# Kernel optimization log

Measured on AMD Instinct MI355X. Metric: run time of the kernel, lower is better.

## Reference

```python
import jax, jax.numpy as jnp
import numpy as np

N_NODES = 50000
N_EDGES = 800000
D_FEAT = 128
HIDDEN = 256
N_CLASSES = 2


def setup_inputs() -> dict:
    key = jax.random.key(0)
    ks = jax.random.split(key, 9)
    x = jax.random.normal(ks[0], (N_NODES, D_FEAT), dtype=jnp.float32)
    edge_index = jax.random.randint(ks[1], (2, N_EDGES), 0, N_NODES, dtype=jnp.int32)
    # SAGEConv params: lin_l (applied to aggregated neighbors), lin_r (root), bias
    s1 = 1.0 / np.sqrt(D_FEAT)
    s2 = 1.0 / np.sqrt(HIDDEN)
    W1l = jax.random.normal(ks[2], (D_FEAT, HIDDEN), dtype=jnp.float32) * s1
    W1r = jax.random.normal(ks[3], (D_FEAT, HIDDEN), dtype=jnp.float32) * s1
    b1 = jax.random.normal(ks[4], (HIDDEN,), dtype=jnp.float32) * s1
    W2l = jax.random.normal(ks[5], (HIDDEN, N_CLASSES), dtype=jnp.float32) * s2
    W2r = jax.random.normal(ks[6], (HIDDEN, N_CLASSES), dtype=jnp.float32) * s2
    b2 = jax.random.normal(ks[7], (N_CLASSES,), dtype=jnp.float32) * s2
    return {"x": x, "edge_index": edge_index, "W1l": W1l, "W1r": W1r,
            "b1": b1, "W2l": W2l, "W2r": W2r, "b2": b2}


def _sage_conv(x, src, dst, Wl, Wr, b):
    # mean-aggregate neighbor features x[src] into destination nodes
    n = x.shape[0]
    agg = jax.ops.segment_sum(x[src], dst, num_segments=n)  # [N, d]
    deg = jax.ops.segment_sum(jnp.ones((src.shape[0],), x.dtype), dst,
                              num_segments=n)
    mean = agg / jnp.maximum(deg, 1.0)[:, None]
    return mean @ Wl + x @ Wr + b


def reference(x, edge_index, W1l, W1r, b1, W2l, W2r, b2):
    src, dst = edge_index[0], edge_index[1]
    h = jax.nn.relu(_sage_conv(x, src, dst, W1l, W1r, b1))
    embeddings = h  # dropout is identity in eval mode
    out = jax.nn.sigmoid(_sage_conv(embeddings, src, dst, W2l, W2r, b2))
    return out, embeddings
```

## Files before the change

### kernel.cpp

```cpp
#include <hip/hip_runtime.h>
#include <math.h>

#define N_NODES 50000
#define N_EDGES 800000
#define D_FEAT 128
#define HIDDEN 256
#define NB_SCAN 196
#define GEMM_BLOCKS 1563

#define PREP_CVT_B 512
#define PREP_WF_B 64
#define AGG_B 2048

#define NSLICE 64
#define SLICE_E 12500
#define NPART 8
#define PART_N 6250

typedef __bf16 bf16x8 __attribute__((ext_vector_type(8)));
typedef float f32x4 __attribute__((ext_vector_type(4)));

__device__ __forceinline__ unsigned f2b(float f) {
    unsigned u = __builtin_bit_cast(unsigned, f);
    return (u + 0x7fff + ((u >> 16) & 1)) >> 16;
}

__global__ __launch_bounds__(256) void prep(
    const float* __restrict__ x,
    const float* __restrict__ W1l, const float* __restrict__ W1r,
    unsigned* __restrict__ xb, unsigned short* __restrict__ Wfrag) {
    int b = blockIdx.x;
    int t = threadIdx.x;
    if (b < PREP_CVT_B) {
        for (int g = b * 256 + t; g < 800000; g += PREP_CVT_B * 256) {
            float4 v0 = *(const float4*)(x + (size_t)g * 8);
            float4 v1 = *(const float4*)(x + (size_t)g * 8 + 4);
            uint4 o;
            o.x = f2b(v0.x) | (f2b(v0.y) << 16);
            o.y = f2b(v0.z) | (f2b(v0.w) << 16);
            o.z = f2b(v1.x) | (f2b(v1.y) << 16);
            o.w = f2b(v1.z) | (f2b(v1.w) << 16);
            int d = g >> 4;
            int j = (g & 15) << 2;
            *(uint4*)(xb + (size_t)d * 64 + j) = o;
        }
    } else {
        for (int tt = (b - PREP_CVT_B) * 256 + t; tt < 65536; tt += PREP_WF_B * 256) {
            int j = tt & 7;
            int lane = (tt >> 3) & 63;
            int ks = (tt >> 9) & 7;
            int nt = tt >> 12;
            int k = ks * 32 + ((lane >> 4) << 3) + j;
            int n = (nt << 4) + (lane & 15);
            float v = (k < 128) ? W1l[k * 256 + n] : W1r[(k - 128) * 256 + n];
            Wfrag[tt] = (unsigned short)f2b(v);
        }
    }
}

__global__ __launch_bounds__(1024) void hist_kernel(const int* __restrict__ dst,
                                                    unsigned* __restrict__ arr) {
    __shared__ unsigned hist[25000];
    int i = blockIdx.x;
    int t = threadIdx.x;
    for (int k = t; k < 25000; k += 1024) hist[k] = 0;
    __syncthreads();
    int e0 = i * SLICE_E;
    for (int k = t; k < SLICE_E; k += 1024) {
        int d = dst[e0 + k];
        atomicAdd(&hist[d >> 1], (d & 1) ? 65536u : 1u);
    }
    __syncthreads();
    for (int d = t; d < N_NODES; d += 1024)
        arr[(size_t)i * N_NODES + d] = (hist[d >> 1] >> ((d & 1) << 4)) & 0xffffu;
}

__global__ void scan1(const unsigned* __restrict__ arr, int* __restrict__ cnt,
                      int* __restrict__ bsum) {
    __shared__ int tmp[256];
    int t = threadIdx.x;
    int i = blockIdx.x * 256 + t;
    int c = 0;
    if (i < N_NODES) {
        for (int k = 0; k < NSLICE; k++) c += (int)arr[(size_t)k * N_NODES + i];
        cnt[i] = c;
    }
    tmp[t] = c;
    __syncthreads();
    for (int off = 128; off > 0; off >>= 1) {
        if (t < off) tmp[t] += tmp[t + off];
        __syncthreads();
    }
    if (t == 0) bsum[blockIdx.x] = tmp[0];
}

__global__ void scanB(const int* __restrict__ cnt, const int* __restrict__ bsum,
                      int* __restrict__ rowbeg, unsigned* __restrict__ arr) {
    __shared__ int bs[256];
    __shared__ int tmp[256];
    int t = threadIdx.x;
    int b = blockIdx.x;
    bs[t] = (t < NB_SCAN) ? bsum[t] : 0;
    __syncthreads();
    for (int off = 1; off < 256; off <<= 1) {
        int y = (t >= off) ? bs[t - off] : 0;
        __syncthreads();
        bs[t] += y;
        __syncthreads();
    }
    int boff = (b == 0) ? 0 : bs[b - 1];
    int i = b * 256 + t;
    int v = (i < N_NODES) ? cnt[i] : 0;
    tmp[t] = v;
    __syncthreads();
    for (int off = 1; off < 256; off <<= 1) {
        int y = (t >= off) ? tmp[t - off] : 0;
        __syncthreads();
        tmp[t] += y;
        __syncthreads();
    }
    if (i < N_NODES) {
        unsigned running = (unsigned)(tmp[t] - v + boff);
        rowbeg[i] = (int)running;
#pragma unroll 4
        for (int k = 0; k < NSLICE; k++) {
            unsigned old = arr[(size_t)k * N_NODES + i];
            arr[(size_t)k * N_NODES + i] = running;
            running += old;
        }
    }
}

__global__ __launch_bounds__(256) void scatter_kernel(
    const int* __restrict__ src, const int* __restrict__ dst,
    const unsigned* __restrict__ arr, unsigned short* __restrict__ esrc) {
    __shared__ unsigned off[PART_N];
    int g = blockIdx.x & 7;
    int i = blockIdx.x >> 3;
    int t = threadIdx.x;
    int lo = g * PART_N;
    for (int k = t; k < PART_N; k += 256)
        off[k] = arr[(size_t)i * N_NODES + lo + k];
    __syncthreads();
    int e0 = i * SLICE_E;
    for (int k = t; k < SLICE_E; k += 256) {
        int e = e0 + k;
        int d = dst[e];
        unsigned dl = (unsigned)(d - lo);
        if (dl < (unsigned)PART_N) {
            unsigned pos = atomicAdd(&off[dl], 1u);
            esrc[pos] = (unsigned short)src[e];
        }
    }
}

__global__ __launch_bounds__(256) void agg1(
    const unsigned* __restrict__ xb, unsigned* __restrict__ mb,
    const unsigned short* __restrict__ esrc,
    const int* __restrict__ rowbeg, const int* __restrict__ cnt) {
    int wid = (blockIdx.x * 256 + threadIdx.x) >> 6;
    int lane = threadIdx.x & 63;
    int g = lane >> 4;
    int i = lane & 15;
    for (int d = wid; d < N_NODES; d += AGG_B * 4) {
        int beg = rowbeg[d];
        int c = cnt[d];
        int end = beg + c;
        float acc[8];
#pragma unroll
        for (int f = 0; f < 8; f++) acc[f] = 0.0f;

        for (int base = beg; base < end; base += 64) {
            int m = end - base; if (m > 64) m = 64;
            int idx = base + lane;
            int e = (int)esrc[idx < end ? idx : end - 1];
            for (int j0 = 0; j0 < m; j0 += 4) {
                int ss = __shfl(e, j0 + g);
                float sc = (j0 + g < m) ? 1.0f : 0.0f;
                uint4 u = *(const uint4*)(xb + (size_t)ss * 64 + (i << 2));
                acc[0] += sc * __builtin_bit_cast(float, u.x << 16);
                acc[1] += sc * __builtin_bit_cast(float, u.x & 0xffff0000u);
                acc[2] += sc * __builtin_bit_cast(float, u.y << 16);
                acc[3] += sc * __builtin_bit_cast(float, u.y & 0xffff0000u);
                acc[4] += sc * __builtin_bit_cast(float, u.z << 16);
                acc[5] += sc * __builtin_bit_cast(float, u.z & 0xffff0000u);
                acc[6] += sc * __builtin_bit_cast(float, u.w << 16);
                acc[7] += sc * __builtin_bit_cast(float, u.w & 0xffff0000u);
            }
        }
#pragma unroll
        for (int f = 0; f < 8; f++) {
            acc[f] += __shfl_xor(acc[f], 16);
            acc[f] += __shfl_xor(acc[f], 32);
        }
        if (lane < 16) {
            float inv = 1.0f / fmaxf((float)c, 1.0f);
            uint4 o;
            o.x = f2b(acc[0] * inv) | (f2b(acc[1] * inv) << 16);
            o.y = f2b(acc[2] * inv) | (f2b(acc[3] * inv) << 16);
            o.z = f2b(acc[4] * inv) | (f2b(acc[5] * inv) << 16);
            o.w = f2b(acc[6] * inv) | (f2b(acc[7] * inv) << 16);
            *(uint4*)(mb + (size_t)d * 64 + (i << 2)) = o;
        }
    }
}

__global__ __launch_bounds__(256) void gemm1ps(
    const unsigned* __restrict__ mb, const unsigned* __restrict__ xb,
    const unsigned short* __restrict__ Wfrag, const float* __restrict__ b1,
    const float* __restrict__ W2l, const float* __restrict__ W2r,
    const float* __restrict__ b2,
    float* __restrict__ h, float* __restrict__ p, float* __restrict__ s) {
    __shared__ unsigned A[32 * 128];
    __shared__ float ppart[32][4];

    int r0 = blockIdx.x * 32;
    int tid = threadIdx.x;
    int w = tid >> 6;
    int lane = tid & 63;
    int quad = lane >> 4;
    int l15 = lane & 15;

    if (tid < 128) ((float*)ppart)[tid] = 0.0f;

    int sr = tid >> 3;
    int c0 = tid & 7;
#pragma unroll
    for (int j = 0; j < 4; j++) {
        int c = c0 + (j << 3);
        uint4 v;
        if (c < 16) v = *(const uint4*)(mb + (size_t)(r0 + sr) * 64 + (c << 2));
        else        v = *(const uint4*)(xb + (size_t)(r0 + sr) * 64 + ((c - 16) << 2));
        int cp = c ^ (sr & 7);
        *(uint4*)(A + sr * 128 + (cp << 2)) = v;
    }
    __syncthreads();

    f32x4 acc[8];
#pragma unroll
    for (int i = 0; i < 8; i++) acc[i] = (f32x4){0.0f, 0.0f, 0.0f, 0.0f};

    for (int ks = 0; ks < 8; ks++) {
        bf16x8 bfr[4];
#pragma unroll
        for (int nt = 0; nt < 4; nt++) {
            int ntg = (w << 2) + nt;
            uint4 raw = *(const uint4*)(Wfrag + ((((ntg << 3) + ks) << 6) + lane) * 8);
            bfr[nt] = __builtin_bit_cast(bf16x8, raw);
        }
#pragma unroll
        for (int mt = 0; mt < 2; mt++) {
            int row = (mt << 4) + l15;
            int c = (ks << 2) + quad;
            uint4 araw = *(const uint4*)(A + row * 128 + ((c ^ (row & 7)) << 2));
            bf16x8 afr = __builtin_bit_cast(bf16x8, araw);
#pragma unroll
            for (int nt = 0; nt < 4; nt++) {
                acc[(mt << 2) + nt] = __builtin_amdgcn_mfma_f32_16x16x32_bf16(
                    afr, bfr[nt], acc[(mt << 2) + nt], 0, 0, 0);
            }
        }
    }

    float w2[4][4];
#pragma unroll
    for (int nt = 0; nt < 4; nt++) {
        int col = (w << 6) + (nt << 4) + l15;
        float2 l2 = *(const float2*)(W2l + col * 2);
        float2 r2 = *(const float2*)(W2r + col * 2);
        w2[nt][0] = l2.x; w2[nt][1] = l2.y; w2[nt][2] = r2.x; w2[nt][3] = r2.y;
    }

#pragma unroll
    for (int mt = 0; mt < 2; mt++) {
        float red[4][4];
#pragma unroll
        for (int v = 0; v < 4; v++)
#pragma unroll
            for (int r = 0; r < 4; r++) red[v][r] = 0.0f;

#pragma unroll
        for (int nt = 0; nt < 4; nt++) {
            int col = (w << 6) + (nt << 4) + l15;
            float b = b1[col];
            f32x4 v = acc[(mt << 2) + nt];
#pragma unroll
            for (int r = 0; r < 4; r++) {
                float hv = v[r] + b;
                hv = hv > 0.0f ? hv : 0.0f;
                int row = r0 + (mt << 4) + (quad << 2) + r;
                if (row < N_NODES)
                    __builtin_nontemporal_store(hv, &h[(size_t)row * 256 + col]);
                red[0][r] += hv * w2[nt][0];
                red[1][r] += hv * w2[nt][1];
                red[2][r] += hv * w2[nt][2];
                red[3][r] += hv * w2[nt][3];
            }
        }
#pragma unroll
        for (int v = 0; v < 4; v++)
#pragma unroll
            for (int r = 0; r < 4; r++) {
                red[v][r] += __shfl_xor(red[v][r], 1);
                red[v][r] += __shfl_xor(red[v][r], 2);
                red[v][r] += __shfl_xor(red[v][r], 4);
                red[v][r] += __shfl_xor(red[v][r], 8);
            }
        if (l15 == 0) {
            int lrow = (mt << 4) + (quad << 2);
#pragma unroll
            for (int r = 0; r < 4; r++)
#pragma unroll
                for (int v = 0; v < 4; v++)
                    atomicAdd(&ppart[lrow + r][v], red[v][r]);
        }
    }
    __syncthreads();

    if (tid < 32) {
        int row = r0 + tid;
        if (row < N_NODES) {
            float2 pv = {ppart[tid][0], ppart[tid][1]};
            float2 sv = {ppart[tid][2] + b2[0], ppart[tid][3] + b2[1]};
            *(float2*)(p + (size_t)row * 2) = pv;
            *(float2*)(s + (size_t)row * 2) = sv;
        }
    }
}

__global__ __launch_bounds__(256) void agg2(
    const float* __restrict__ p, const float* __restrict__ s,
    const unsigned short* __restrict__ esrc,
    const int* __restrict__ rowbeg, const int* __restrict__ cnt,
    float* __restrict__ out) {
    int wid = (blockIdx.x * 256 + threadIdx.x) >> 6;
    int lane = threadIdx.x & 63;
    for (int d = wid; d < N_NODES; d += AGG_B * 4) {
        int beg = rowbeg[d];
        int c = cnt[d];
        int end = beg + c;
        float a0 = 0.0f, a1 = 0.0f;
        for (int base = beg; base < end; base += 64) {
            int idx = base + lane;
            if (idx < end) {
                int ss = (int)esrc[idx];
                float2 v = *(const float2*)(p + (size_t)ss * 2);
                a0 += v.x; a1 += v.y;
            }
        }
#pragma unroll
        for (int off = 32; off > 0; off >>= 1) {
            a0 += __shfl_down(a0, off);
            a1 += __shfl_down(a1, off);
        }
        if (lane == 0) {
            float inv = 1.0f / fmaxf((float)c, 1.0f);
            float z0 = a0 * inv + s[(size_t)d * 2 + 0];
            float z1 = a1 * inv + s[(size_t)d * 2 + 1];
            float2 o = {1.0f / (1.0f + expf(-z0)), 1.0f / (1.0f + expf(-z1))};
            *(float2*)(out + (size_t)d * 2) = o;
        }
    }
}

extern "C" void kernel_launch(void* const* d_in, const int* in_sizes, int n_in,
                              void* d_out, int out_size, void* d_ws, size_t ws_size,
                              hipStream_t stream) {
    const float* x   = (const float*)d_in[0];
    const int*   ei  = (const int*)d_in[1];
    const float* W1l = (const float*)d_in[2];
    const float* W1r = (const float*)d_in[3];
    const float* b1  = (const float*)d_in[4];
    const float* W2l = (const float*)d_in[5];
    const float* W2r = (const float*)d_in[6];
    const float* b2  = (const float*)d_in[7];

    const int* src = ei;
    const int* dst = ei + N_EDGES;

    float* out = (float*)d_out;
    float* emb = out + (size_t)N_NODES * 2;

    int* cnt    = (int*)d_ws;
    int* rowbeg = cnt + N_NODES;
    int* bsum   = rowbeg + N_NODES;
    unsigned short* esrc = (unsigned short*)(bsum + 256);
    unsigned* xb = (unsigned*)(esrc + 800064);
    unsigned* mb = xb + (size_t)50048 * 64;
    unsigned* arr = mb;
    unsigned short* Wfrag = (unsigned short*)(mb + (size_t)50048 * 64);
    float* p = (float*)(Wfrag + 65536);
    float* s = p + (size_t)N_NODES * 2;

    prep<<<PREP_CVT_B + PREP_WF_B, 256, 0, stream>>>(x, W1l, W1r, xb, Wfrag);

    hist_kernel<<<NSLICE, 1024, 0, stream>>>(dst, arr);
    scan1<<<NB_SCAN, 256, 0, stream>>>(arr, cnt, bsum);
    scanB<<<NB_SCAN, 256, 0, stream>>>(cnt, bsum, rowbeg, arr);
    scatter_kernel<<<NSLICE * NPART, 256, 0, stream>>>(src, dst, arr, esrc);

    agg1<<<AGG_B, 256, 0, stream>>>(xb, mb, esrc, rowbeg, cnt);

    gemm1ps<<<GEMM_BLOCKS, 256, 0, stream>>>(mb, xb, Wfrag, b1, W2l, W2r, b2,
                                             emb, p, s);

    agg2<<<AGG_B, 256, 0, stream>>>(p, s, esrc, rowbeg, cnt, out);
}
```

Before: 225.9 us.

## Fuse histogram into prep kernel and record per-edge ranks for atomic-free scatter

The dst histogram now runs inside the prep kernel as 512 partitioned tasks (slice × node-partition), each with a small shared-memory histogram. These blocks sit alongside the conversion blocks, which replaces the separate 64-block hist kernel with its large shared array. The atomicAdd return value is kept as a per-edge rank in scratch space reused from the embedding output. This lets the scatter become a simple per-edge kernel with no atomics or partition filtering. In exchange, every partition block rereads its slice of dst (8x redundant reads), and the rank buffer adds extra traffic.

Result: no change. 223.0 us (-1.3%).

```diff
diff --git a/kernel.cpp b/kernel.cpp
--- a/kernel.cpp
+++ b/kernel.cpp
@@ -8,14 +8,16 @@
 #define NB_SCAN 196
 #define GEMM_BLOCKS 1563
 
-#define PREP_CVT_B 512
-#define PREP_WF_B 64
 #define AGG_B 2048
 
 #define NSLICE 64
 #define SLICE_E 12500
 #define NPART 8
 #define PART_N 6250
+#define NTASK 512
+
+#define PH_B 1024
+#define SCAT_B 3125
 
 typedef __bf16 bf16x8 __attribute__((ext_vector_type(8)));
 typedef float f32x4 __attribute__((ext_vector_type(4)));
@@ -25,14 +27,36 @@
     return (u + 0x7fff + ((u >> 16) & 1)) >> 16;
 }
 
-__global__ __launch_bounds__(256) void prep(
-    const float* __restrict__ x,
+__global__ __launch_bounds__(256) void prep_hist(
+    const float* __restrict__ x, const int* __restrict__ dst,
     const float* __restrict__ W1l, const float* __restrict__ W1r,
+    unsigned* __restrict__ arr, unsigned short* __restrict__ rank,
     unsigned* __restrict__ xb, unsigned short* __restrict__ Wfrag) {
+    __shared__ unsigned hist[PART_N / 2 + 11];
     int b = blockIdx.x;
     int t = threadIdx.x;
-    if (b < PREP_CVT_B) {
-        for (int g = b * 256 + t; g < 800000; g += PREP_CVT_B * 256) {
+    if (b < NTASK) {
+        int slice = b >> 3, part = b & 7;
+        int lo = part * PART_N;
+        for (int k = t; k < PART_N / 2; k += 256) hist[k] = 0;
+        __syncthreads();
+        int e0 = slice * SLICE_E;
+        for (int k = t; k < SLICE_E; k += 256) {
+            int e = e0 + k;
+            int d = dst[e];
+            unsigned dl = (unsigned)(d - lo);
+            if (dl < (unsigned)PART_N) {
+                unsigned old = atomicAdd(&hist[dl >> 1], (dl & 1) ? 65536u : 1u);
+                rank[e] = (unsigned short)((old >> ((dl & 1) << 4)) & 0xffffu);
+            }
+        }
+        __syncthreads();
+        for (int k = t; k < PART_N; k += 256)
+            arr[(size_t)slice * N_NODES + lo + k] =
+                (hist[k >> 1] >> ((k & 1) << 4)) & 0xffffu;
+    } else {
+        int cb = b - NTASK;
+        for (int g = cb * 256 + t; g < 800000; g += NTASK * 256) {
             float4 v0 = *(const float4*)(x + (size_t)g * 8);
             float4 v1 = *(const float4*)(x + (size_t)g * 8 + 4);
             uint4 o;
@@ -44,8 +68,7 @@
             int j = (g & 15) << 2;
             *(uint4*)(xb + (size_t)d * 64 + j) = o;
         }
-    } else {
-        for (int tt = (b - PREP_CVT_B) * 256 + t; tt < 65536; tt += PREP_WF_B * 256) {
+        for (int tt = cb * 256 + t; tt < 65536; tt += NTASK * 256) {
             int j = tt & 7;
             int lane = (tt >> 3) & 63;
             int ks = (tt >> 9) & 7;
@@ -56,23 +79,6 @@
             Wfrag[tt] = (unsigned short)f2b(v);
         }
     }
-}
-
-__global__ __launch_bounds__(1024) void hist_kernel(const int* __restrict__ dst,
-                                                    unsigned* __restrict__ arr) {
-    __shared__ unsigned hist[25000];
-    int i = blockIdx.x;
-    int t = threadIdx.x;
-    for (int k = t; k < 25000; k += 1024) hist[k] = 0;
-    __syncthreads();
-    int e0 = i * SLICE_E;
-    for (int k = t; k < SLICE_E; k += 1024) {
-        int d = dst[e0 + k];
-        atomicAdd(&hist[d >> 1], (d & 1) ? 65536u : 1u);
-    }
-    __syncthreads();
-    for (int d = t; d < N_NODES; d += 1024)
-        arr[(size_t)i * N_NODES + d] = (hist[d >> 1] >> ((d & 1) << 4)) & 0xffffu;
 }
 
 __global__ void scan1(const unsigned* __restrict__ arr, int* __restrict__ cnt,
@@ -131,26 +137,16 @@
     }
 }
 
-__global__ __launch_bounds__(256) void scatter_kernel(
+__global__ __launch_bounds__(256) void scatter2(
     const int* __restrict__ src, const int* __restrict__ dst,
-    const unsigned* __restrict__ arr, unsigned short* __restrict__ esrc) {
-    __shared__ unsigned off[PART_N];
-    int g = blockIdx.x & 7;
-    int i = blockIdx.x >> 3;
-    int t = threadIdx.x;
-    int lo = g * PART_N;
-    for (int k = t; k < PART_N; k += 256)
-        off[k] = arr[(size_t)i * N_NODES + lo + k];
-    __syncthreads();
-    int e0 = i * SLICE_E;
-    for (int k = t; k < SLICE_E; k += 256) {
-        int e = e0 + k;
+    const unsigned* __restrict__ arr, const unsigned short* __restrict__ rank,
+    unsigned short* __restrict__ esrc) {
+    int e = blockIdx.x * 256 + threadIdx.x;
+    if (e < N_EDGES) {
+        int slice = e / SLICE_E;
         int d = dst[e];
-        unsigned dl = (unsigned)(d - lo);
-        if (dl < (unsigned)PART_N) {
-            unsigned pos = atomicAdd(&off[dl], 1u);
-            esrc[pos] = (unsigned short)src[e];
-        }
+        unsigned pos = arr[(size_t)slice * N_NODES + d] + (unsigned)rank[e];
+        esrc[pos] = (unsigned short)src[e];
     }
 }
 
@@ -391,13 +387,12 @@
     unsigned short* Wfrag = (unsigned short*)(mb + (size_t)50048 * 64);
     float* p = (float*)(Wfrag + 65536);
     float* s = p + (size_t)N_NODES * 2;
-
-    prep<<<PREP_CVT_B + PREP_WF_B, 256, 0, stream>>>(x, W1l, W1r, xb, Wfrag);
-
-    hist_kernel<<<NSLICE, 1024, 0, stream>>>(dst, arr);
+    unsigned short* rank = (unsigned short*)emb;
+
+    prep_hist<<<PH_B, 256, 0, stream>>>(x, dst, W1l, W1r, arr, rank, xb, Wfrag);
     scan1<<<NB_SCAN, 256, 0, stream>>>(arr, cnt, bsum);
     scanB<<<NB_SCAN, 256, 0, stream>>>(cnt, bsum, rowbeg, arr);
-    scatter_kernel<<<NSLICE * NPART, 256, 0, stream>>>(src, dst, arr, esrc);
+    scatter2<<<SCAT_B, 256, 0, stream>>>(src, dst, arr, rank, esrc);
 
     agg1<<<AGG_B, 256, 0, stream>>>(xb, mb, esrc, rowbeg, cnt);
 
```
